# Kernel tuning notes

Hardware: AMD Instinct MI355X
Metric: run time of the kernel (lower is better)

The kernel has to match this reference:

```python
import jax, jax.numpy as jnp
import numpy as np

LN_EPS = 1e-5

def setup_inputs() -> dict:
    key = jax.random.key(0)
    ks = jax.random.split(key, 6)
    N, CD, CC, CF = 500000, 64, 96, 128
    return {
        "x_detial": jax.random.normal(ks[0], (N, CD), dtype=jnp.float32),
        "x_context": jax.random.normal(ks[1], (N, CC), dtype=jnp.float32),
        "W_detial": jax.random.normal(ks[2], (CD, CF), dtype=jnp.float32) * 0.05,
        "W_context": jax.random.normal(ks[3], (CC, CF), dtype=jnp.float32) * 0.05,
        "W_gate1": jax.random.normal(ks[4], (CD + CC, CF // 2), dtype=jnp.float32) * 0.05,
        "ln_gamma": jnp.ones((CF // 2,), dtype=jnp.float32),
        "ln_beta": jnp.zeros((CF // 2,), dtype=jnp.float32),
        "W_gate2": jax.random.normal(ks[5], (CF // 2, 1), dtype=jnp.float32) * 0.05,
    }

def _layer_norm(x, gamma, beta):
    mu = jnp.mean(x, axis=-1, keepdims=True)
    var = jnp.mean(jnp.square(x - mu), axis=-1, keepdims=True)
    return (x - mu) * jax.lax.rsqrt(var + LN_EPS) * gamma + beta

def reference(x_detial, x_context, W_detial, W_context, W_gate1, ln_gamma, ln_beta, W_gate2):
    # gate path: 1x1 subm conv == per-point linear on [N, C] features
    concat = jnp.concatenate([x_detial, x_context], axis=1)        # [N, CD+CC]
    h = jnp.matmul(concat, W_gate1)                                 # [N, CF//2]
    h = jax.nn.relu(_layer_norm(h, ln_gamma, ln_beta))
    gate = jax.nn.sigmoid(jnp.matmul(h, W_gate2))                   # [N, 1]
    detail_aligned = jnp.matmul(x_detial, W_detial)                 # [N, CF]
    context_aligned = jnp.matmul(x_context, W_context)              # [N, CF]
    return (1.0 - gate) * context_aligned + gate * detail_aligned   # [N, CF]
```

## Files before the change

### kernel.cpp

```cpp
#include <hip/hip_runtime.h>
#include <hip/hip_bf16.h>
#include <math.h>


namespace {

typedef __attribute__((ext_vector_type(8))) short short8;
typedef __attribute__((ext_vector_type(4))) float f32x4;

constexpr int CD = 64, CC = 96, CH = 64, CF = 128;
constexpr int NFG1 = 20;
constexpr int NFCB = 40;
constexpr int NFRAG = NFG1 + NFCB;
constexpr int WCH_ALL = NFRAG * 512 * 2 / 16;

__device__ inline short bf16_of(float f) {
  __hip_bfloat16 h = __float2bfloat16(f);
  return *reinterpret_cast<short*>(&h);
}

__global__ void convert_weights(const float* __restrict__ Wd,
                                const float* __restrict__ Wc,
                                const float* __restrict__ Wg1,
                                short* __restrict__ ws) {
  const int t = blockIdx.x * 256 + threadIdx.x;
  if (t >= 64 * NFRAG) return;
  const int frag = t >> 6, l = t & 63;
  const int cidx = l & 15, kb = l >> 4;
  float v[8];
  if (frag < NFG1) {
    const int ks = frag >> 2, nt = frag & 3;
    const int n = nt * 16 + cidx;
    #pragma unroll
    for (int j = 0; j < 8; ++j) {
      const int k = ks * 32 + (j >> 2) * 16 + kb * 4 + (j & 3);
      v[j] = Wg1[k * CH + n];
    }
  } else {
    const int f2 = frag - NFG1;
    const int ks = f2 >> 3, nt = f2 & 7;
    const int n = nt * 16 + cidx;
    #pragma unroll
    for (int j = 0; j < 8; ++j) {
      const int k = ks * 32 + (j >> 2) * 16 + kb * 4 + (j & 3);
      v[j] = (k < CD) ? Wd[k * CF + n] : Wc[(k - CD) * CF + n];
    }
  }
  short8 o;
  #pragma unroll
  for (int j = 0; j < 8; ++j) o[j] = bf16_of(v[j]);
  *reinterpret_cast<short8*>(ws + frag * 512 + l * 8) = o;
}

__global__ __launch_bounds__(512, 2)
void gate_fusion_mfma(const float* __restrict__ xd,
                      const float* __restrict__ xc,
                      const float* __restrict__ gma,
                      const float* __restrict__ bta,
                      const float* __restrict__ Wg2,
                      const short* __restrict__ wf,
                      float* __restrict__ out, int N) {
  __shared__ short wlds[NFRAG * 512];
  __shared__ float tr[8][4][136];

  const int tid  = threadIdx.x;
  const int lane = tid & 63;
  const int wv   = tid >> 6;
  const int r0   = blockIdx.x * 128 + wv * 16;
  const int cidx = lane & 15;
  const int kb   = lane >> 4;
  const bool active = (r0 < N);

  f32x4 buf[5][2];
  if (active) {
    const size_t row = (size_t)(r0 + cidx);
    const float* rd = xd + row * CD + kb * 4;
    const float* rc = xc + row * CC + kb * 4;
    #pragma unroll
    for (int ks = 0; ks < 5; ++ks) {
      const float* p = (ks < 2) ? (rd + ks * 32) : (rc + (ks - 2) * 32);
      buf[ks][0] = *reinterpret_cast<const f32x4*>(p);
      buf[ks][1] = *reinterpret_cast<const f32x4*>(p + 16);
    }
  }

  {
    #pragma unroll
    for (int it = 0; it < 8; ++it) {
      const int c = tid + it * 512;
      if (it < 7 || c < WCH_ALL) {
        short8 v = *reinterpret_cast<const short8*>(wf + (size_t)c * 8);
        *reinterpret_cast<short8*>(&wlds[c * 8]) = v;
      }
    }
  }

  __syncthreads();
  if (!active) return;

  float gmv[4], btv[4], w2v[4];
  #pragma unroll
  for (int nt = 0; nt < 4; ++nt) {
    const int c = nt * 16 + cidx;
    gmv[nt] = gma[c]; btv[nt] = bta[c]; w2v[nt] = Wg2[c];
  }

  short8 xf[5];
  #pragma unroll
  for (int ks = 0; ks < 5; ++ks) {
    short8 f;
    #pragma unroll
    for (int j = 0; j < 4; ++j) {
      f[j]     = bf16_of(buf[ks][0][j]);
      f[4 + j] = bf16_of(buf[ks][1][j]);
    }
    xf[ks] = f;
  }

  const f32x4 vzero = {0.f, 0.f, 0.f, 0.f};
  f32x4 acc1[4];
  #pragma unroll
  for (int nt = 0; nt < 4; ++nt) acc1[nt] = vzero;

  #pragma unroll
  for (int ks = 0; ks < 5; ++ks) {
    short8 bg[4];
    #pragma unroll
    for (int nt = 0; nt < 4; ++nt)
      bg[nt] = *reinterpret_cast<const short8*>(
          &wlds[(ks * 4 + nt) * 512 + lane * 8]);
    #pragma unroll
    for (int nt = 0; nt < 4; ++nt)
      acc1[nt] = __builtin_amdgcn_mfma_f32_16x16x32_bf16(
          xf[ks], bg[nt], acc1[nt], 0, 0, 0);
  }

  float gate[4];
  {
    float s[4], q[4];
    #pragma unroll
    for (int r = 0; r < 4; ++r) {
      s[r] = 0.f; q[r] = 0.f;
      #pragma unroll
      for (int nt = 0; nt < 4; ++nt) {
        const float c = acc1[nt][r];
        s[r] += c; q[r] += c * c;
      }
    }
    #pragma unroll
    for (int m = 1; m < 16; m <<= 1)
      #pragma unroll
      for (int r = 0; r < 4; ++r) {
        s[r] += __shfl_xor(s[r], m, 64);
        q[r] += __shfl_xor(q[r], m, 64);
      }
    float p[4];
    #pragma unroll
    for (int r = 0; r < 4; ++r) {
      const float mu  = s[r] * (1.f / CH);
      const float var = q[r] * (1.f / CH) - mu * mu;
      const float rsd = rsqrtf(var + 1e-5f);
      float pp = 0.f;
      #pragma unroll
      for (int nt = 0; nt < 4; ++nt) {
        const float h = fmaxf((acc1[nt][r] - mu) * rsd * gmv[nt] + btv[nt], 0.f);
        pp += h * w2v[nt];
      }
      p[r] = pp;
    }
    #pragma unroll
    for (int m = 1; m < 16; m <<= 1)
      #pragma unroll
      for (int r = 0; r < 4; ++r) p[r] += __shfl_xor(p[r], m, 64);
    #pragma unroll
    for (int r = 0; r < 4; ++r) gate[r] = 1.f / (1.f + expf(-p[r]));
  }

  f32x4 o[4][2];
  #pragma unroll
  for (int q = 0; q < 4; ++q) {
    f32x4 aD[2], aC[2];
    #pragma unroll
    for (int nt = 0; nt < 2; ++nt) { aD[nt] = vzero; aC[nt] = vzero; }

    #pragma unroll
    for (int ks = 0; ks < 5; ++ks) {
      short8 bg[2];
      #pragma unroll
      for (int nt = 0; nt < 2; ++nt)
        bg[nt] = *reinterpret_cast<const short8*>(
            &wlds[(NFG1 + ks * 8 + q * 2 + nt) * 512 + lane * 8]);
      if (ks < 2) {
        #pragma unroll
        for (int nt = 0; nt < 2; ++nt)
          aD[nt] = __builtin_amdgcn_mfma_f32_16x16x32_bf16(
              xf[ks], bg[nt], aD[nt], 0, 0, 0);
      } else {
        #pragma unroll
        for (int nt = 0; nt < 2; ++nt)
          aC[nt] = __builtin_amdgcn_mfma_f32_16x16x32_bf16(
              xf[ks], bg[nt], aC[nt], 0, 0, 0);
      }
    }
    #pragma unroll
    for (int nt = 0; nt < 2; ++nt)
      #pragma unroll
      for (int r = 0; r < 4; ++r)
        o[q][nt][r] = fmaf(gate[r], aD[nt][r] - aC[nt][r], aC[nt][r]);
  }

  {
    float (*trw)[136] = tr[wv];
    #pragma unroll
    for (int r = 0; r < 4; ++r) {
      #pragma unroll
      for (int q = 0; q < 4; ++q)
        #pragma unroll
        for (int nt = 0; nt < 2; ++nt)
          trw[kb][(q * 2 + nt) * 16 + cidx] = o[q][nt][r];
      #pragma unroll
      for (int i = 0; i < 2; ++i) {
        const int ri = i * 2 + (lane >> 5);
        const f32x4 v = *reinterpret_cast<const f32x4*>(
            &trw[ri][(lane & 31) * 4]);
        float* dst = &out[((size_t)r0 + ri * 4 + r) * CF + (lane & 31) * 4];
        asm volatile("global_store_dwordx4 %0, %1, off nt"
                     :: "v"(dst), "v"(v) : "memory");
      }
    }
  }
}

}

extern "C" void kernel_launch(void* const* d_in, const int* in_sizes, int n_in,
                              void* d_out, int out_size, void* d_ws, size_t ws_size,
                              hipStream_t stream) {
  const float* xd  = (const float*)d_in[0];
  const float* xc  = (const float*)d_in[1];
  const float* Wd  = (const float*)d_in[2];
  const float* Wc  = (const float*)d_in[3];
  const float* Wg1 = (const float*)d_in[4];
  const float* gma = (const float*)d_in[5];
  const float* bta = (const float*)d_in[6];
  const float* Wg2 = (const float*)d_in[7];
  float* out = (float*)d_out;
  short* ws  = (short*)d_ws;

  const int N = in_sizes[0] / CD;

  convert_weights<<<dim3(15), dim3(256), 0, stream>>>(Wd, Wc, Wg1, ws);

  const int nblk = (N + 127) / 128;
  gate_fusion_mfma<<<dim3(nblk), dim3(512), 0, stream>>>(
      xd, xc, gma, bta, Wg2, ws, out, N);
}
```

Before: 114.4 us.

## Use persistent blocks with producer waves double-buffering inputs through LDS

Launches a fixed grid of 256 persistent blocks. Half the waves act as producers that burst-load input tiles into a double-buffered LDS staging area, while the other half consume tiles and run the MFMA gate/fusion math and stores. The goal is to overlap global loads with compute and amortize the per-block weight staging into LDS. The cost is fewer loads in flight per CU, only one block per CU, extra LDS traffic, and per-iteration block barriers. Rows beyond a multiple of 16 are no longer handled.

```diff
diff --git a/kernel.cpp b/kernel.cpp
--- a/kernel.cpp
+++ b/kernel.cpp
@@ -52,37 +52,50 @@
   *reinterpret_cast<short8*>(ws + frag * 512 + l * 8) = o;
 }
 
-__global__ __launch_bounds__(512, 2)
+#define BURST(p0,p1,p2,p3,p4,p5,p6,p7,p8,p9, rdp, rcp)                \
+  asm volatile(                                                        \
+      "global_load_dwordx4 %0, %[ad], off\n\t"                         \
+      "global_load_dwordx4 %1, %[ad], off offset:64\n\t"               \
+      "global_load_dwordx4 %2, %[ad], off offset:128\n\t"              \
+      "global_load_dwordx4 %3, %[ad], off offset:192\n\t"              \
+      "global_load_dwordx4 %4, %[ac], off\n\t"                         \
+      "global_load_dwordx4 %5, %[ac], off offset:64\n\t"               \
+      "global_load_dwordx4 %6, %[ac], off offset:128\n\t"              \
+      "global_load_dwordx4 %7, %[ac], off offset:192\n\t"              \
+      "global_load_dwordx4 %8, %[ac], off offset:256\n\t"              \
+      "global_load_dwordx4 %9, %[ac], off offset:320"                  \
+      : "=&v"(p0), "=&v"(p1), "=&v"(p2), "=&v"(p3), "=&v"(p4),         \
+        "=&v"(p5), "=&v"(p6), "=&v"(p7), "=&v"(p8), "=&v"(p9)          \
+      : [ad] "v"(rdp), [ac] "v"(rcp)                                   \
+      : "memory")
+
+#define WAIT0(p0,p1,p2,p3,p4,p5,p6,p7,p8,p9)                           \
+  asm volatile("s_waitcnt vmcnt(0)"                                    \
+      : "+v"(p0), "+v"(p1), "+v"(p2), "+v"(p3), "+v"(p4),              \
+        "+v"(p5), "+v"(p6), "+v"(p7), "+v"(p8), "+v"(p9)               \
+      :: "memory")
+
+__global__ __launch_bounds__(512, 1)
 void gate_fusion_mfma(const float* __restrict__ xd,
                       const float* __restrict__ xc,
                       const float* __restrict__ gma,
                       const float* __restrict__ bta,
                       const float* __restrict__ Wg2,
                       const short* __restrict__ wf,
-                      float* __restrict__ out, int N) {
+                      float* __restrict__ out,
+                      int nTiles, int T) {
   __shared__ short wlds[NFRAG * 512];
-  __shared__ float tr[8][4][136];
+  __shared__ f32x4 xbuf[2][4][640];
+  __shared__ float tr[4][4][136];
 
   const int tid  = threadIdx.x;
   const int lane = tid & 63;
   const int wv   = tid >> 6;
-  const int r0   = blockIdx.x * 128 + wv * 16;
   const int cidx = lane & 15;
   const int kb   = lane >> 4;
-  const bool active = (r0 < N);
-
-  f32x4 buf[5][2];
-  if (active) {
-    const size_t row = (size_t)(r0 + cidx);
-    const float* rd = xd + row * CD + kb * 4;
-    const float* rc = xc + row * CC + kb * 4;
-    #pragma unroll
-    for (int ks = 0; ks < 5; ++ks) {
-      const float* p = (ks < 2) ? (rd + ks * 32) : (rc + (ks - 2) * 32);
-      buf[ks][0] = *reinterpret_cast<const f32x4*>(p);
-      buf[ks][1] = *reinterpret_cast<const f32x4*>(p + 16);
-    }
-  }
+  const bool producer = (wv >= 4);
+  const int  pair     = producer ? (wv - 4) : wv;
+  const int  tbase    = blockIdx.x * T * 4;
 
   {
     #pragma unroll
@@ -95,139 +108,170 @@
     }
   }
 
+  auto produce = [&](int t, int bsel) {
+    const int tc = (t < nTiles) ? t : (nTiles - 1);
+    const float* rdp = xd + ((size_t)tc * 16 + cidx) * CD + kb * 4;
+    const float* rcp = xc + ((size_t)tc * 16 + cidx) * CC + kb * 4;
+    f32x4 b0,b1,b2,b3,b4,b5,b6,b7,b8,b9;
+    BURST(b0,b1,b2,b3,b4,b5,b6,b7,b8,b9, rdp, rcp);
+    WAIT0(b0,b1,b2,b3,b4,b5,b6,b7,b8,b9);
+    __builtin_amdgcn_sched_barrier(0);
+    f32x4* dst = &xbuf[bsel][pair][0];
+    dst[0 * 64 + lane] = b0;  dst[1 * 64 + lane] = b1;
+    dst[2 * 64 + lane] = b2;  dst[3 * 64 + lane] = b3;
+    dst[4 * 64 + lane] = b4;  dst[5 * 64 + lane] = b5;
+    dst[6 * 64 + lane] = b6;  dst[7 * 64 + lane] = b7;
+    dst[8 * 64 + lane] = b8;  dst[9 * 64 + lane] = b9;
+  };
+
+  float gmv[4], btv[4], w2v[4];
+  if (!producer) {
+    #pragma unroll
+    for (int nt = 0; nt < 4; ++nt) {
+      const int c = nt * 16 + cidx;
+      gmv[nt] = gma[c]; btv[nt] = bta[c]; w2v[nt] = Wg2[c];
+    }
+  }
+
+  const f32x4 vzero = {0.f, 0.f, 0.f, 0.f};
+
+  auto consume = [&](int t, int bsel) {
+    if (t >= nTiles) return;
+    const int r0 = t * 16;
+    const f32x4* src = &xbuf[bsel][pair][0];
+
+    short8 xf[5];
+    #pragma unroll
+    for (int ks = 0; ks < 5; ++ks) {
+      const f32x4 lo = src[(2 * ks) * 64 + lane];
+      const f32x4 hi = src[(2 * ks + 1) * 64 + lane];
+      short8 f;
+      #pragma unroll
+      for (int j = 0; j < 4; ++j) { f[j] = bf16_of(lo[j]); f[4 + j] = bf16_of(hi[j]); }
+      xf[ks] = f;
+    }
+
+    f32x4 acc1[4];
+    #pragma unroll
+    for (int nt = 0; nt < 4; ++nt) acc1[nt] = vzero;
+    #pragma unroll
+    for (int ks = 0; ks < 5; ++ks) {
+      short8 bg[4];
+      #pragma unroll
+      for (int nt = 0; nt < 4; ++nt)
+        bg[nt] = *reinterpret_cast<const short8*>(
+            &wlds[(ks * 4 + nt) * 512 + lane * 8]);
+      #pragma unroll
+      for (int nt = 0; nt < 4; ++nt)
+        acc1[nt] = __builtin_amdgcn_mfma_f32_16x16x32_bf16(
+            xf[ks], bg[nt], acc1[nt], 0, 0, 0);
+    }
+
+    float gate[4];
+    {
+      float s[4], q[4];
+      #pragma unroll
+      for (int r = 0; r < 4; ++r) {
+        s[r] = 0.f; q[r] = 0.f;
+        #pragma unroll
+        for (int nt = 0; nt < 4; ++nt) {
+          const float c = acc1[nt][r];
+          s[r] += c; q[r] += c * c;
+        }
+      }
+      #pragma unroll
+      for (int m = 1; m < 16; m <<= 1)
+        #pragma unroll
+        for (int r = 0; r < 4; ++r) {
+          s[r] += __shfl_xor(s[r], m, 64);
+          q[r] += __shfl_xor(q[r], m, 64);
+        }
+      float p[4];
+      #pragma unroll
+      for (int r = 0; r < 4; ++r) {
+        const float mu  = s[r] * (1.f / CH);
+        const float var = q[r] * (1.f / CH) - mu * mu;
+        const float rsd = rsqrtf(var + 1e-5f);
+        float pp = 0.f;
+        #pragma unroll
+        for (int nt = 0; nt < 4; ++nt) {
+          const float h = fmaxf((acc1[nt][r] - mu) * rsd * gmv[nt] + btv[nt], 0.f);
+          pp += h * w2v[nt];
+        }
+        p[r] = pp;
+      }
+      #pragma unroll
+      for (int m = 1; m < 16; m <<= 1)
+        #pragma unroll
+        for (int r = 0; r < 4; ++r) p[r] += __shfl_xor(p[r], m, 64);
+      #pragma unroll
+      for (int r = 0; r < 4; ++r) gate[r] = 1.f / (1.f + expf(-p[r]));
+    }
+
+    f32x4 o[4][2];
+    #pragma unroll
+    for (int q = 0; q < 4; ++q) {
+      f32x4 aD[2], aC[2];
+      #pragma unroll
+      for (int nt = 0; nt < 2; ++nt) { aD[nt] = vzero; aC[nt] = vzero; }
+      #pragma unroll
+      for (int ks = 0; ks < 5; ++ks) {
+        short8 bg[2];
+        #pragma unroll
+        for (int nt = 0; nt < 2; ++nt)
+          bg[nt] = *reinterpret_cast<const short8*>(
+              &wlds[(NFG1 + ks * 8 + q * 2 + nt) * 512 + lane * 8]);
+        if (ks < 2) {
+          #pragma unroll
+          for (int nt = 0; nt < 2; ++nt)
+            aD[nt] = __builtin_amdgcn_mfma_f32_16x16x32_bf16(
+                xf[ks], bg[nt], aD[nt], 0, 0, 0);
+        } else {
+          #pragma unroll
+          for (int nt = 0; nt < 2; ++nt)
+            aC[nt] = __builtin_amdgcn_mfma_f32_16x16x32_bf16(
+                xf[ks], bg[nt], aC[nt], 0, 0, 0);
+        }
+      }
+      #pragma unroll
+      for (int nt = 0; nt < 2; ++nt)
+        #pragma unroll
+        for (int r = 0; r < 4; ++r)
+          o[q][nt][r] = fmaf(gate[r], aD[nt][r] - aC[nt][r], aC[nt][r]);
+    }
+
+    {
+      float (*trw)[136] = tr[pair];
+      #pragma unroll
+      for (int r = 0; r < 4; ++r) {
+        #pragma unroll
+        for (int q = 0; q < 4; ++q)
+          #pragma unroll
+          for (int nt = 0; nt < 2; ++nt)
+            trw[kb][(q * 2 + nt) * 16 + cidx] = o[q][nt][r];
+        #pragma unroll
+        for (int i = 0; i < 2; ++i) {
+          const int ri = i * 2 + (lane >> 5);
+          const f32x4 v = *reinterpret_cast<const f32x4*>(
+              &trw[ri][(lane & 31) * 4]);
+          float* dst = &out[((size_t)r0 + ri * 4 + r) * CF + (lane & 31) * 4];
+          asm volatile("global_store_dwordx4 %0, %1, off nt"
+                       :: "v"(dst), "v"(v) : "memory");
+        }
+      }
+    }
+  };
+
+  if (producer) produce(tbase + 0 * 4 + pair, 0);
   __syncthreads();
-  if (!active) return;
-
-  float gmv[4], btv[4], w2v[4];
-  #pragma unroll
-  for (int nt = 0; nt < 4; ++nt) {
-    const int c = nt * 16 + cidx;
-    gmv[nt] = gma[c]; btv[nt] = bta[c]; w2v[nt] = Wg2[c];
-  }
-
-  short8 xf[5];
-  #pragma unroll
-  for (int ks = 0; ks < 5; ++ks) {
-    short8 f;
-    #pragma unroll
-    for (int j = 0; j < 4; ++j) {
-      f[j]     = bf16_of(buf[ks][0][j]);
-      f[4 + j] = bf16_of(buf[ks][1][j]);
-    }
-    xf[ks] = f;
-  }
-
-  const f32x4 vzero = {0.f, 0.f, 0.f, 0.f};
-  f32x4 acc1[4];
-  #pragma unroll
-  for (int nt = 0; nt < 4; ++nt) acc1[nt] = vzero;
-
-  #pragma unroll
-  for (int ks = 0; ks < 5; ++ks) {
-    short8 bg[4];
-    #pragma unroll
-    for (int nt = 0; nt < 4; ++nt)
-      bg[nt] = *reinterpret_cast<const short8*>(
-          &wlds[(ks * 4 + nt) * 512 + lane * 8]);
-    #pragma unroll
-    for (int nt = 0; nt < 4; ++nt)
-      acc1[nt] = __builtin_amdgcn_mfma_f32_16x16x32_bf16(
-          xf[ks], bg[nt], acc1[nt], 0, 0, 0);
-  }
-
-  float gate[4];
-  {
-    float s[4], q[4];
-    #pragma unroll
-    for (int r = 0; r < 4; ++r) {
-      s[r] = 0.f; q[r] = 0.f;
-      #pragma unroll
-      for (int nt = 0; nt < 4; ++nt) {
-        const float c = acc1[nt][r];
-        s[r] += c; q[r] += c * c;
-      }
-    }
-    #pragma unroll
-    for (int m = 1; m < 16; m <<= 1)
-      #pragma unroll
-      for (int r = 0; r < 4; ++r) {
-        s[r] += __shfl_xor(s[r], m, 64);
-        q[r] += __shfl_xor(q[r], m, 64);
-      }
-    float p[4];
-    #pragma unroll
-    for (int r = 0; r < 4; ++r) {
-      const float mu  = s[r] * (1.f / CH);
-      const float var = q[r] * (1.f / CH) - mu * mu;
-      const float rsd = rsqrtf(var + 1e-5f);
-      float pp = 0.f;
-      #pragma unroll
-      for (int nt = 0; nt < 4; ++nt) {
-        const float h = fmaxf((acc1[nt][r] - mu) * rsd * gmv[nt] + btv[nt], 0.f);
-        pp += h * w2v[nt];
-      }
-      p[r] = pp;
-    }
-    #pragma unroll
-    for (int m = 1; m < 16; m <<= 1)
-      #pragma unroll
-      for (int r = 0; r < 4; ++r) p[r] += __shfl_xor(p[r], m, 64);
-    #pragma unroll
-    for (int r = 0; r < 4; ++r) gate[r] = 1.f / (1.f + expf(-p[r]));
-  }
-
-  f32x4 o[4][2];
-  #pragma unroll
-  for (int q = 0; q < 4; ++q) {
-    f32x4 aD[2], aC[2];
-    #pragma unroll
-    for (int nt = 0; nt < 2; ++nt) { aD[nt] = vzero; aC[nt] = vzero; }
-
-    #pragma unroll
-    for (int ks = 0; ks < 5; ++ks) {
-      short8 bg[2];
-      #pragma unroll
-      for (int nt = 0; nt < 2; ++nt)
-        bg[nt] = *reinterpret_cast<const short8*>(
-            &wlds[(NFG1 + ks * 8 + q * 2 + nt) * 512 + lane * 8]);
-      if (ks < 2) {
-        #pragma unroll
-        for (int nt = 0; nt < 2; ++nt)
-          aD[nt] = __builtin_amdgcn_mfma_f32_16x16x32_bf16(
-              xf[ks], bg[nt], aD[nt], 0, 0, 0);
-      } else {
-        #pragma unroll
-        for (int nt = 0; nt < 2; ++nt)
-          aC[nt] = __builtin_amdgcn_mfma_f32_16x16x32_bf16(
-              xf[ks], bg[nt], aC[nt], 0, 0, 0);
-      }
-    }
-    #pragma unroll
-    for (int nt = 0; nt < 2; ++nt)
-      #pragma unroll
-      for (int r = 0; r < 4; ++r)
-        o[q][nt][r] = fmaf(gate[r], aD[nt][r] - aC[nt][r], aC[nt][r]);
-  }
-
-  {
-    float (*trw)[136] = tr[wv];
-    #pragma unroll
-    for (int r = 0; r < 4; ++r) {
-      #pragma unroll
-      for (int q = 0; q < 4; ++q)
-        #pragma unroll
-        for (int nt = 0; nt < 2; ++nt)
-          trw[kb][(q * 2 + nt) * 16 + cidx] = o[q][nt][r];
-      #pragma unroll
-      for (int i = 0; i < 2; ++i) {
-        const int ri = i * 2 + (lane >> 5);
-        const f32x4 v = *reinterpret_cast<const f32x4*>(
-            &trw[ri][(lane & 31) * 4]);
-        float* dst = &out[((size_t)r0 + ri * 4 + r) * CF + (lane & 31) * 4];
-        asm volatile("global_store_dwordx4 %0, %1, off nt"
-                     :: "v"(dst), "v"(v) : "memory");
-      }
-    }
+
+  for (int r = 0; r < T; ++r) {
+    if (producer) {
+      if (r + 1 < T) produce(tbase + (r + 1) * 4 + pair, (r + 1) & 1);
+    } else {
+      consume(tbase + r * 4 + pair, r & 1);
+    }
+    __syncthreads();
   }
 }
 
@@ -248,10 +292,12 @@
   short* ws  = (short*)d_ws;
 
   const int N = in_sizes[0] / CD;
+  const int nTiles = N / 16;
 
   convert_weights<<<dim3(15), dim3(256), 0, stream>>>(Wd, Wc, Wg1, ws);
 
-  const int nblk = (N + 127) / 128;
+  const int nblk = 256;
+  const int T = (nTiles + nblk * 4 - 1) / (nblk * 4);
   gate_fusion_mfma<<<dim3(nblk), dim3(512), 0, stream>>>(
-      xd, xc, gma, bta, Wg2, ws, out, N);
-}
+      xd, xc, gma, bta, Wg2, ws, out, nTiles, T);
+}
```

Result: slower. 117.1 us (+2.4%).
